# Performance work log

Hardware: AMD Instinct MI355X
Metric: run time of the kernel (lower is better)

Reference implementation:

```python
import jax, jax.numpy as jnp
from jax import lax
import numpy as np

SQRT2 = 1.4142135623730951
STYLE_DIM = 512
MOD_SCALE = 1.0 / np.sqrt(float(STYLE_DIM))          # EqualLinear modulation, lr_mul=1
MAP_SCALE = 0.01 / np.sqrt(float(STYLE_DIM))          # mapping EqualLinear, lr_mul=0.01
LR_MUL = 0.01


def _blur_kernel():
    k = np.array([1.0, 3.0, 3.0, 1.0], dtype=np.float32)
    k = k[None, :] * k[:, None]
    return jnp.asarray(k / k.sum())


def upfirdn2d(x, k, up=1, down=1, pad=(0, 0)):
    # torch upfirdn2d inserts (up-1) zeros AFTER each sample -> extra trailing pad of up-1
    C = x.shape[1]
    kern = jnp.tile(k[None, None], (C, 1, 1, 1))  # depthwise [C,1,kh,kw] (kernel symmetric, no flip needed)
    p = (pad[0], pad[1] + up - 1)
    return lax.conv_general_dilated(x, kern, (down, down), [p, p], lhs_dilation=(up, up),
                                    dimension_numbers=('NCHW', 'OIHW', 'NCHW'), feature_group_count=C)


def fused_lrelu(x, b):
    return jax.nn.leaky_relu(x + b.reshape(1, -1, 1, 1), 0.2) * SQRT2


def grouped_conv(x, w, pad, up):
    # x: [B,I,H,W], w: [B,O,I,k,k] per-sample weights -> grouped conv with B groups
    B, O, I, kh, kw = w.shape
    xg = x.reshape(1, B * I, x.shape[2], x.shape[3])
    if up:
        # torch conv_transpose2d(stride=2, padding=0) == dilated conv with spatially flipped kernel
        wf = jnp.flip(w, (-2, -1)).reshape(B * O, I, kh, kw)
        out = lax.conv_general_dilated(xg, wf, (1, 1), [(kh - 1, kh - 1), (kw - 1, kw - 1)],
                                       lhs_dilation=(2, 2),
                                       dimension_numbers=('NCHW', 'OIHW', 'NCHW'), feature_group_count=B)
    else:
        out = lax.conv_general_dilated(xg, w.reshape(B * O, I, kh, kw), (1, 1), [(pad, pad), (pad, pad)],
                                       dimension_numbers=('NCHW', 'OIHW', 'NCHW'), feature_group_count=B)
    return out.reshape(B, O, out.shape[2], out.shape[3])


def mod_conv(x, weight, style, mod_w, mod_b, demodulate, up, blur_k):
    # weight: [O,I,k,k]; style: [B,512]
    s = style @ (mod_w * MOD_SCALE).T + mod_b                       # [B,I]
    scale = 1.0 / np.sqrt(float(weight.shape[1] * weight.shape[2] * weight.shape[3]))
    w = scale * weight[None] * s[:, None, :, None, None]            # [B,O,I,k,k]
    if demodulate:
        d = lax.rsqrt(jnp.sum(w * w, axis=(2, 3, 4)) + 1e-8)
        w = w * d[:, :, None, None, None]
    out = grouped_conv(x, w, weight.shape[-1] // 2, up)
    if up:
        out = upfirdn2d(out, blur_k * 4.0, pad=(1, 1))              # Blur pad from p=len(k)-2-(3-1)=0
    return out


def _forward(z, mlp_w, mlp_b, const_input, conv_w, conv_mod_w, conv_mod_b, conv_bias,
             noise_strength, rgb_w, rgb_mod_w, rgb_mod_b, rgb_bias):
    B = z.shape[0]
    blur_k = _blur_kernel()
    w_lat = z * lax.rsqrt(jnp.mean(z * z, axis=1, keepdims=True) + 1e-8)
    for i in range(mlp_w.shape[0]):
        w_lat = jax.nn.leaky_relu(w_lat @ (mlp_w[i] * MAP_SCALE).T + mlp_b[i] * LR_MUL, 0.2) * SQRT2
    nkey = jax.random.key(7)

    def noise(l, shape):
        return jax.random.normal(jax.random.fold_in(nkey, l), (shape[0], 1, shape[2], shape[3]), dtype=jnp.float32)

    def styled(x, l, up):
        y = mod_conv(x, conv_w[l], w_lat, conv_mod_w[l], conv_mod_b[l], True, up, blur_k)
        y = y + noise_strength[l] * noise(l, y.shape)
        return fused_lrelu(y, conv_bias[l])

    def to_rgb(x, i):
        y = mod_conv(x, rgb_w[i], w_lat, rgb_mod_w[i], rgb_mod_b[i], False, False, blur_k)
        return y + rgb_bias[i].reshape(1, -1, 1, 1)

    out = jnp.tile(const_input, (B, 1, 1, 1))   # ConstantInput (shift=0 -> identity rolls)
    out = styled(out, 0, False)
    skip = to_rgb(out, 0)
    l = 1
    for blk in range(3):  # resolutions 8, 16, 32
        out = styled(out, l, True); l += 1
        out = styled(out, l, False); l += 1
        # Upsample(skip): kernel*factor^2, pad=(2,1), up=2
        skip = to_rgb(out, blk + 1) + upfirdn2d(skip, blur_k * 4.0, up=2, pad=(2, 1))
    return skip  # [B,3,32,32]


def setup_inputs() -> dict:
    key = jax.random.key(0)
    ks = jax.random.split(key, 8)
    B, S, C = 8, 512, 512
    return {
        'z': jax.random.normal(ks[0], (B, S), jnp.float32),
        'mlp_w': jax.random.normal(ks[1], (8, S, S), jnp.float32),
        'mlp_b': jnp.zeros((8, S), jnp.float32),
        'const_input': jax.random.normal(ks[2], (1, C, 4, 4), jnp.float32),
        'conv_w': jax.random.normal(ks[3], (7, C, C, 3, 3), jnp.float32),
        'conv_mod_w': jax.random.normal(ks[4], (7, C, S), jnp.float32),
        'conv_mod_b': jnp.ones((7, C), jnp.float32),
        'conv_bias': jnp.zeros((7, C), jnp.float32),
        'noise_strength': jax.random.normal(ks[5], (7,), jnp.float32) * 0.1,
        'rgb_w': jax.random.normal(ks[6], (4, 3, C, 1, 1), jnp.float32),
        'rgb_mod_w': jax.random.normal(ks[7], (4, C, S), jnp.float32),
        'rgb_mod_b': jnp.ones((4, C), jnp.float32),
        'rgb_bias': jnp.zeros((4, 3), jnp.float32),
    }


def reference(z, mlp_w, mlp_b, const_input, conv_w, conv_mod_w, conv_mod_b, conv_bias,
              noise_strength, rgb_w, rgb_mod_w, rgb_mod_b, rgb_bias):
    return _forward(z, mlp_w, mlp_b, const_input, conv_w, conv_mod_w, conv_mod_b, conv_bias,
                    noise_strength, rgb_w, rgb_mod_w, rgb_mod_b, rgb_bias)
```

## Files before the change

### kernel.cpp

```cpp
#include <hip/hip_runtime.h>


#define SQRT2F      1.41421356f
#define MAP_SCALE   4.41941738e-04f
#define MOD_SCALE   4.41941738e-02f
#define CONV_SCALE  1.47313913e-02f
#define RGB_SCALE   4.41941738e-02f

typedef __attribute__((ext_vector_type(8))) short bf16x8;
typedef __attribute__((ext_vector_type(16))) float f32x16;

__device__ __forceinline__ float bf2f(ushort u) {
    return __uint_as_float(((unsigned)u) << 16);
}
__device__ __forceinline__ ushort f2bf(float f) {
    unsigned u = __float_as_uint(f);
    unsigned r = (u + 0x7FFFu + ((u >> 16) & 1u)) >> 16;
    return (ushort)r;
}
__device__ __forceinline__ void store4bf(ushort* p, float a, float b, float c, float d) {
    union { ushort u[4]; uint2 v; } x;
    x.u[0] = f2bf(a); x.u[1] = f2bf(b); x.u[2] = f2bf(c); x.u[3] = f2bf(d);
    *(uint2*)p = x.v;
}

typedef __attribute__((address_space(1))) const unsigned int GAS;
typedef __attribute__((address_space(3))) unsigned int LAS;
__device__ __forceinline__ void gload_lds16(const ushort* g, ushort* l) {
    __builtin_amdgcn_global_load_lds((GAS*)g, (LAS*)l, 16, 0, 0);
}


__device__ __forceinline__ unsigned rotl32(unsigned x, int r) {
    return (x << r) | (x >> (32 - r));
}

__device__ void threefry2x32(unsigned k0, unsigned k1, unsigned x0, unsigned x1,
                             unsigned& o0, unsigned& o1) {
    unsigned k2 = k0 ^ k1 ^ 0x1BD11BDAu;
    x0 += k0; x1 += k1;
    x0 += x1; x1 = rotl32(x1,13); x1 ^= x0;
    x0 += x1; x1 = rotl32(x1,15); x1 ^= x0;
    x0 += x1; x1 = rotl32(x1,26); x1 ^= x0;
    x0 += x1; x1 = rotl32(x1, 6); x1 ^= x0;
    x0 += k1; x1 += k2 + 1u;
    x0 += x1; x1 = rotl32(x1,17); x1 ^= x0;
    x0 += x1; x1 = rotl32(x1,29); x1 ^= x0;
    x0 += x1; x1 = rotl32(x1,16); x1 ^= x0;
    x0 += x1; x1 = rotl32(x1,24); x1 ^= x0;
    x0 += k2; x1 += k0 + 2u;
    x0 += x1; x1 = rotl32(x1,13); x1 ^= x0;
    x0 += x1; x1 = rotl32(x1,15); x1 ^= x0;
    x0 += x1; x1 = rotl32(x1,26); x1 ^= x0;
    x0 += x1; x1 = rotl32(x1, 6); x1 ^= x0;
    x0 += k0; x1 += k1 + 3u;
    x0 += x1; x1 = rotl32(x1,17); x1 ^= x0;
    x0 += x1; x1 = rotl32(x1,29); x1 ^= x0;
    x0 += x1; x1 = rotl32(x1,16); x1 ^= x0;
    x0 += x1; x1 = rotl32(x1,24); x1 ^= x0;
    x0 += k1; x1 += k2 + 4u;
    x0 += x1; x1 = rotl32(x1,13); x1 ^= x0;
    x0 += x1; x1 = rotl32(x1,15); x1 ^= x0;
    x0 += x1; x1 = rotl32(x1,26); x1 ^= x0;
    x0 += x1; x1 = rotl32(x1, 6); x1 ^= x0;
    x0 += k2; x1 += k0 + 5u;
    o0 = x0; o1 = x1;
}

__device__ float bits_to_normal(unsigned bits) {
    unsigned m = (bits >> 9) | 0x3F800000u;
    float f = __uint_as_float(m) - 1.0f;
    const float lo = -0.99999994f;
    float u = f * 2.0f + lo;
    u = fmaxf(lo, u);
    float w = -log1pf(-u * u);
    float p;
    if (w < 5.0f) {
        w -= 2.5f;
        p = 2.81022636e-08f;
        p = fmaf(p, w, 3.43273939e-07f);
        p = fmaf(p, w, -3.5233877e-06f);
        p = fmaf(p, w, -4.39150654e-06f);
        p = fmaf(p, w, 0.00021858087f);
        p = fmaf(p, w, -0.00125372503f);
        p = fmaf(p, w, -0.00417768164f);
        p = fmaf(p, w, 0.246640727f);
        p = fmaf(p, w, 1.50140941f);
    } else {
        w = sqrtf(w) - 3.0f;
        p = -0.000200214257f;
        p = fmaf(p, w, 0.000100950558f);
        p = fmaf(p, w, 0.00134934322f);
        p = fmaf(p, w, -0.00367342844f);
        p = fmaf(p, w, 0.00573950773f);
        p = fmaf(p, w, -0.0076224613f);
        p = fmaf(p, w, 0.00943887047f);
        p = fmaf(p, w, 1.00167406f);
        p = fmaf(p, w, 2.83297682f);
    }
    return 1.41421354f * (p * u);
}

__global__ void noise_kernel(float* __restrict__ nbuf) {
    int g = blockIdx.x * 256 + threadIdx.x;
    if (g >= 21632) return;
    const int off[8] = {0, 128, 640, 1152, 3200, 5248, 13440, 21632};
    int l = 0;
    while (l < 6 && g >= off[l + 1]) l++;
    int i = g - off[l];
    unsigned k0, k1;
    threefry2x32(0u, 7u, 0u, (unsigned)l, k0, k1);
    unsigned b0, b1;
    threefry2x32(k0, k1, 0u, (unsigned)i, b0, b1);
    nbuf[g] = bits_to_normal(b0 ^ b1);
}


__global__ void pixelnorm_kernel(const float* __restrict__ z, float* __restrict__ out) {
    int b = blockIdx.x;
    int lane = threadIdx.x;
    float v[8];
    float s = 0.f;
    #pragma unroll
    for (int j = 0; j < 8; j++) {
        v[j] = z[b * 512 + lane + (j << 6)];
        s += v[j] * v[j];
    }
    #pragma unroll
    for (int off = 32; off > 0; off >>= 1) s += __shfl_xor(s, off, 64);
    float norm = rsqrtf(s * (1.f / 512.f) + 1e-8f);
    #pragma unroll
    for (int j = 0; j < 8; j++)
        out[b * 512 + lane + (j << 6)] = v[j] * norm;
}

__global__ void dot512_kernel(const float* __restrict__ win, const float* __restrict__ W,
                              const float* __restrict__ bias, float* __restrict__ out,
                              int total, float wscale, float bscale, int mode) {
    int gt = blockIdx.x * blockDim.x + threadIdx.x;
    int wv = gt >> 6;
    int lane = gt & 63;
    if (wv >= total) return;
    int l = wv >> 12;
    int r = wv & 4095;
    int b = r >> 9;
    int o = r & 511;
    const float* wrow = W + ((size_t)(l * 512 + o) << 9);
    const float* xrow = win + ((size_t)b << 9);
    float s = 0.f;
    #pragma unroll
    for (int j = 0; j < 8; j++) {
        int k = lane + (j << 6);
        s += wrow[k] * xrow[k];
    }
    #pragma unroll
    for (int off = 32; off > 0; off >>= 1) s += __shfl_xor(s, off, 64);
    if (lane == 0) {
        float v = s * wscale + bias[l * 512 + o] * bscale;
        if (mode) v = (v > 0.f ? v : 0.2f * v) * SQRT2F;
        out[wv] = v;
    }
}

__global__ void wbconv_all(const float* __restrict__ cw, ushort* __restrict__ wb7,
                           float* __restrict__ wsq7) {
    int gid = blockIdx.x * 256 + threadIdx.x;
    if (gid >= 7 * 262144) return;
    int l = gid >> 18;
    int idx = gid & 262143;
    int o = idx >> 9, i = idx & 511;
    int flip = (l == 1 || l == 3 || l == 5);
    const float* p = cw + (size_t)gid * 9;
    float w9[9];
    float s = 0.f;
    #pragma unroll
    for (int t = 0; t < 9; t++) { w9[t] = p[t]; s += w9[t] * w9[t]; }
    wsq7[gid] = s;
    ushort* wb = wb7 + (size_t)l * 2359296;
    #pragma unroll
    for (int t = 0; t < 9; t++) {
        int tsrc = flip ? (8 - t) : t;
        wb[((size_t)(t * 512 + o) << 9) + i] = f2bf(w9[tsrc]);
    }
}

__global__ void demod_all(const float* __restrict__ wsq7, const float* __restrict__ sc,
                          float* __restrict__ dm) {
    int gt = blockIdx.x * blockDim.x + threadIdx.x;
    int wv = gt >> 6;
    int lane = gt & 63;
    if (wv >= 7 * 4096) return;
    int l = wv >> 12, b = (wv >> 9) & 7, o = wv & 511;
    const float* wr = wsq7 + (size_t)l * 262144 + ((size_t)o << 9);
    const float* sr = sc + l * 4096 + (b << 9);
    float s = 0.f;
    #pragma unroll
    for (int j = 0; j < 8; j++) {
        int k = lane + (j << 6);
        float sv = sr[k];
        s += wr[k] * sv * sv;
    }
    #pragma unroll
    for (int off = 32; off > 0; off >>= 1) s += __shfl_xor(s, off, 64);
    if (lane == 0) dm[wv] = rsqrtf(s * (1.f / 4608.f) + 1e-8f);
}

__global__ void prep0_kernel(const float* __restrict__ cinp, const float* __restrict__ s0,
                             ushort* __restrict__ X0p) {
    int gid = blockIdx.x * 256 + threadIdx.x;
    if (gid >= 8 * 36 * 64) return;
    int grp = gid & 63;
    int r = gid >> 6;
    int b = r / 36, rc = r % 36, row = rc / 6, col = rc % 6;
    int y = row - 1, x = col - 1;
    union { ushort u[8]; bf16x8 v; } pk;
    if (y >= 0 && y < 4 && x >= 0 && x < 4) {
        #pragma unroll
        for (int k = 0; k < 8; k++) {
            int ch = grp * 8 + k;
            pk.u[k] = f2bf(cinp[ch * 16 + y * 4 + x] * s0[b * 512 + ch]);
        }
    } else {
        #pragma unroll
        for (int k = 0; k < 8; k++) pk.u[k] = 0;
    }
    *(bf16x8*)&X0p[(((size_t)(b * 6 + row) * 6 + col) << 9) + grp * 8] = pk.v;
}

template <int S, int NTILE, int WROWS, int KS, bool WUP>
__global__ __launch_bounds__(256, 2) void conv_dense4(
    const ushort* __restrict__ Xp, const ushort* __restrict__ wb,
    const float* __restrict__ dm, const float* __restrict__ nz,
    const float* __restrict__ nstr, const float* __restrict__ bias,
    const float* __restrict__ snext,
    ushort* __restrict__ T, ushort* __restrict__ XU, float* __restrict__ Pp) {
    constexpr int SP = S + 2, P2 = S * S, N = 8 * P2;
    constexpr int JCOLS = NTILE / 128;
    constexpr int NPX = WROWS * SP;
    constexpr int ASZ = 9 * 4 * 64 * 8;
    constexpr int BSZ = NPX * 32;
    constexpr int PAIR = ASZ + BSZ;
    constexpr int NBU = NPX * 4;
    constexpr int NBT = (NBU + 255) / 256;
    constexpr int ROWMAX = 8 * SP - 1;
    constexpr int CK = 16 / KS;
    constexpr int DB = (CK > 1) ? 2 : 1;
    constexpr int MINB = (NBU > 192) ? ((NBU - 192 + 255) / 256) : 0;
    constexpr int NMIN = 9 + MINB;
    __shared__ __align__(16) ushort lds[DB * PAIR];

    const int tid = threadIdx.x, lane = tid & 63, nw = tid >> 6;
    const int hf = lane >> 5, l31 = lane & 31;
    const int o0 = blockIdx.x * 64;
    const int n0 = blockIdx.y * NTILE;
    const int ks = blockIdx.z;
    const int R0 = (n0 / P2) * SP + (n0 % P2) / S;
    const int ao = tid & 63, ai = tid >> 6;

    int pixbase[JCOLS], nj[JCOLS];
    #pragma unroll
    for (int j = 0; j < JCOLS; j++) {
        int n = n0 + nw * (NTILE / 4) + j * 32 + l31;
        nj[j] = n;
        int b = n / P2, r = n % P2;
        int y = r / S, x = r % S;
        pixbase[j] = (b * SP + y - R0) * SP + x;
    }
    f32x16 acc[JCOLS][2];
    #pragma unroll
    for (int j = 0; j < JCOLS; j++) { acc[j][0] = (f32x16)0.f; acc[j][1] = (f32x16)0.f; }

    int bgo[NBT];
    bool bgv[NBT];
    #pragma unroll
    for (int r = 0; r < NBT; r++) {
        int t = tid + 256 * r;
        bgv[r] = t < NBU;
        int tt = bgv[r] ? t : 0;
        int px = tt % NPX, kv = tt / NPX;
        int rr = px / SP, cc = px % SP;
        int Rc = R0 + rr; if (Rc > ROWMAX) Rc = ROWMAX;
        bgo[r] = ((Rc * SP + cc) << 9) + kv * 8;
    }
    const ushort* wsrc = wb + ((size_t)(o0 + ao) << 9) + ai * 8;
    const int ibase = ks * CK * 32;

    auto stage = [&](int c, int buf) {
        const int i0 = ibase + c * 32;
        ushort* dstA = &lds[buf * PAIR + nw * 512];
        ushort* dstB = &lds[buf * PAIR + ASZ + nw * 512];
        #pragma unroll
        for (int r = 0; r < 9; r++)
            gload_lds16(wsrc + ((size_t)(r * 512) << 9) + i0, dstA + r * 2048);
        #pragma unroll
        for (int r = 0; r < NBT; r++)
            if (bgv[r])
                gload_lds16(Xp + bgo[r] + i0, dstB + r * 2048);
    };

    stage(0, 0);
    for (int c = 0; c < CK; c++) {
        const int cur = c & 1;
        if (c + 1 < CK) {
            stage(c + 1, cur ^ 1);
            asm volatile("s_waitcnt vmcnt(%0)" :: "i"(NMIN) : "memory");
        } else {
            asm volatile("s_waitcnt vmcnt(0)" ::: "memory");
        }
        __builtin_amdgcn_s_barrier();
        __builtin_amdgcn_sched_barrier(0);
        const int bo = cur * PAIR;
        #pragma unroll
        for (int t = 0; t < 9; t++) {
            const int dpx = (t / 3) * SP + (t % 3);
            #pragma unroll
            for (int s = 0; s < 2; s++) {
                const int kv = s * 2 + hf;
                bf16x8 a0 = *(const bf16x8*)&lds[bo + ((t * 4 + kv) * 64 + l31) * 8];
                bf16x8 a1 = *(const bf16x8*)&lds[bo + ((t * 4 + kv) * 64 + 32 + l31) * 8];
                #pragma unroll
                for (int j = 0; j < JCOLS; j++) {
                    bf16x8 bf = *(const bf16x8*)&lds[bo + ASZ + (kv * NPX + pixbase[j] + dpx) * 8];
                    acc[j][0] = __builtin_amdgcn_mfma_f32_32x32x16_bf16(a0, bf, acc[j][0], 0, 0, 0);
                    acc[j][1] = __builtin_amdgcn_mfma_f32_32x32x16_bf16(a1, bf, acc[j][1], 0, 0, 0);
                }
            }
        }
        __builtin_amdgcn_sched_barrier(0);
        __builtin_amdgcn_s_barrier();
    }

    if constexpr (KS > 1) {
        #pragma unroll
        for (int j = 0; j < JCOLS; j++) {
            float* pb = Pp + (((size_t)(ks * N + nj[j])) << 9) + o0;
            #pragma unroll
            for (int sub = 0; sub < 2; sub++) {
                #pragma unroll
                for (int rq = 0; rq < 4; rq++) {
                    float4 v = make_float4(acc[j][sub][rq * 4 + 0], acc[j][sub][rq * 4 + 1],
                                           acc[j][sub][rq * 4 + 2], acc[j][sub][rq * 4 + 3]);
                    *(float4*)&pb[sub * 32 + 4 * hf + 8 * rq] = v;
                }
            }
        }
        return;
    }
    float ns = nstr[0];
    #pragma unroll
    for (int j = 0; j < JCOLS; j++) {
        int n = nj[j], b = n / P2, r = n % P2;
        float nv = nz[b * P2 + r];
        int y = r / S, x = r % S;
        size_t tbase = (size_t)n << 9;
        size_t ubase = ((size_t)(b * SP + y + 1) * SP + x + 1) << 9;
        #pragma unroll
        for (int sub = 0; sub < 2; sub++) {
            #pragma unroll
            for (int rq = 0; rq < 4; rq++) {
                int o = o0 + sub * 32 + 4 * hf + 8 * rq;
                float4 d4 = *(const float4*)&dm[b * 512 + o];
                float4 b4 = *(const float4*)&bias[o];
                float vv[4];
                #pragma unroll
                for (int ri = 0; ri < 4; ri++) {
                    float v = acc[j][sub][rq * 4 + ri] * (&d4.x)[ri] * CONV_SCALE
                              + ns * nv + (&b4.x)[ri];
                    vv[ri] = (v > 0.f ? v : 0.2f * v) * SQRT2F;
                }
                store4bf(T + tbase + o, vv[0], vv[1], vv[2], vv[3]);
                if (WUP) {
                    float4 s4 = *(const float4*)&snext[b * 512 + o];
                    store4bf(XU + ubase + o, vv[0] * s4.x, vv[1] * s4.y,
                             vv[2] * s4.z, vv[3] * s4.w);
                }
            }
        }
    }
}

template <int S, int KS, bool WUP>
__global__ void combine_dense(const float* __restrict__ Pp, const float* __restrict__ dm,
                              const float* __restrict__ nz, const float* __restrict__ nstr,
                              const float* __restrict__ bias, const float* __restrict__ snext,
                              ushort* __restrict__ T, ushort* __restrict__ XU) {
    constexpr int P2 = S * S, N = 8 * P2, SP = S + 2;
    int gid = blockIdx.x * 256 + threadIdx.x;
    int n = gid >> 7, og = (gid & 127) << 2;
    float4 sm = make_float4(0.f, 0.f, 0.f, 0.f);
    #pragma unroll
    for (int k = 0; k < KS; k++) {
        float4 p = *(const float4*)&Pp[(((size_t)(k * N + n)) << 9) + og];
        sm.x += p.x; sm.y += p.y; sm.z += p.z; sm.w += p.w;
    }
    int b = n / P2, r = n % P2;
    float nsv = nstr[0] * nz[b * P2 + r];
    float4 d4 = *(const float4*)&dm[b * 512 + og];
    float4 b4 = *(const float4*)&bias[og];
    float vv[4];
    const float* sp = &sm.x;
    #pragma unroll
    for (int i = 0; i < 4; i++) {
        float v = sp[i] * (&d4.x)[i] * CONV_SCALE + nsv + (&b4.x)[i];
        vv[i] = (v > 0.f ? v : 0.2f * v) * SQRT2F;
    }
    store4bf(&T[((size_t)n << 9) + og], vv[0], vv[1], vv[2], vv[3]);
    if (WUP) {
        int y = r / S, x = r % S;
        float4 s4 = *(const float4*)&snext[b * 512 + og];
        store4bf(&XU[(((size_t)(b * SP + y + 1) * SP + x + 1) << 9) + og],
                 vv[0] * s4.x, vv[1] * s4.y, vv[2] * s4.z, vv[3] * s4.w);
    }
}

template <int HIN, int NTILE, int WRW>
__global__ __launch_bounds__(256, 2) void conv_up4(
    const ushort* __restrict__ Xp, const ushort* __restrict__ wb,
    const float* __restrict__ dm, ushort* __restrict__ U) {
    constexpr int SPI = HIN + 2, SOUT = 2 * HIN + 1, SPO = SOUT + 2;
    constexpr int JCOLS = NTILE / 128;
    constexpr int NPX = WRW * SPI;
    constexpr int ASZ = 4 * 4 * 64 * 8;
    constexpr int BSZ = NPX * 32;
    constexpr int PAIR = ASZ + BSZ;
    constexpr int NBU = NPX * 4;
    constexpr int NBT = (NBU + 255) / 256;
    constexpr int ROWMAX = 8 * SPI - 1;
    constexpr int MINB = (NBU > 192) ? ((NBU - 192 + 255) / 256) : 0;
    constexpr int NMIN = 4 + MINB;
    __shared__ __align__(16) ushort lds[2 * PAIR];

    const int py = blockIdx.z >> 1, pxp = blockIdx.z & 1;
    const int GY = py ? HIN : HIN + 1, GX = pxp ? HIN : HIN + 1;
    const int GG = GY * GX, NCLS = 8 * GG;
    const int NTY = py ? 1 : 2, NTX = pxp ? 1 : 2, NT = NTY * NTX;
    const int n0 = blockIdx.y * NTILE;
    if (n0 >= NCLS) return;

    int taplist[4], toffs[4];
    {
        int k = 0;
        #pragma unroll
        for (int a2 = 0; a2 < 2; a2++) {
            if (a2 >= NTY) break;
            int dy = py ? 1 : a2 * 2;
            #pragma unroll
            for (int c2 = 0; c2 < 2; c2++) {
                if (c2 >= NTX) break;
                int dx = pxp ? 1 : c2 * 2;
                taplist[k] = dy * 3 + dx;
                toffs[k] = ((dy + py) >> 1) * SPI + ((dx + pxp) >> 1);
                k++;
            }
        }
        for (; k < 4; k++) { taplist[k] = 0; toffs[k] = 0; }
    }

    const int tid = threadIdx.x, lane = tid & 63, nw = tid >> 6;
    const int hf = lane >> 5, l31 = lane & 31;
    const int o0 = blockIdx.x * 64;
    const int R0 = (n0 / GG) * SPI + (n0 % GG) / GX;
    const int ao = tid & 63, ai = tid >> 6;

    int pixbase[JCOLS], bj[JCOLS], gyj[JCOLS], gxj[JCOLS];
    bool validj[JCOLS];
    #pragma unroll
    for (int j = 0; j < JCOLS; j++) {
        int n = n0 + nw * (NTILE / 4) + j * 32 + l31;
        validj[j] = n < NCLS;
        int nc = validj[j] ? n : (NCLS - 1);
        int b = nc / GG, rem = nc % GG;
        int gy = rem / GX, gx = rem % GX;
        bj[j] = b; gyj[j] = gy; gxj[j] = gx;
        pixbase[j] = (b * SPI + gy - R0) * SPI + gx;
    }
    f32x16 acc[JCOLS][2];
    #pragma unroll
    for (int j = 0; j < JCOLS; j++) { acc[j][0] = (f32x16)0.f; acc[j][1] = (f32x16)0.f; }

    int bgo[NBT];
    bool bgv[NBT];
    #pragma unroll
    for (int r = 0; r < NBT; r++) {
        int t = tid + 256 * r;
        bgv[r] = t < NBU;
        int tt = bgv[r] ? t : 0;
        int px = tt % NPX, kv = tt / NPX;
        int rr = px / SPI, cc = px % SPI;
        int Rc = R0 + rr; if (Rc > ROWMAX) Rc = ROWMAX;
        bgo[r] = ((Rc * SPI + cc) << 9) + kv * 8;
    }
    const ushort* wsrc = wb + ((size_t)(o0 + ao) << 9) + ai * 8;

    auto stage = [&](int c, int buf) {
        const int i0 = c * 32;
        ushort* dstA = &lds[buf * PAIR + nw * 512];
        ushort* dstB = &lds[buf * PAIR + ASZ + nw * 512];
        #pragma unroll
        for (int r = 0; r < 4; r++)
            gload_lds16(wsrc + ((size_t)(taplist[r] * 512) << 9) + i0, dstA + r * 2048);
        #pragma unroll
        for (int r = 0; r < NBT; r++)
            if (bgv[r])
                gload_lds16(Xp + bgo[r] + i0, dstB + r * 2048);
    };

    stage(0, 0);
    for (int c = 0; c < 16; c++) {
        const int cur = c & 1;
        if (c + 1 < 16) {
            stage(c + 1, cur ^ 1);
            asm volatile("s_waitcnt vmcnt(%0)" :: "i"(NMIN) : "memory");
        } else {
            asm volatile("s_waitcnt vmcnt(0)" ::: "memory");
        }
        __builtin_amdgcn_s_barrier();
        __builtin_amdgcn_sched_barrier(0);
        const int bo = cur * PAIR;
        for (int tt = 0; tt < NT; ++tt) {
            const int dpx = toffs[tt];
            #pragma unroll
            for (int s = 0; s < 2; s++) {
                const int kv = s * 2 + hf;
                bf16x8 a0 = *(const bf16x8*)&lds[bo + ((tt * 4 + kv) * 64 + l31) * 8];
                bf16x8 a1 = *(const bf16x8*)&lds[bo + ((tt * 4 + kv) * 64 + 32 + l31) * 8];
                #pragma unroll
                for (int j = 0; j < JCOLS; j++) {
                    bf16x8 bf = *(const bf16x8*)&lds[bo + ASZ + (kv * NPX + pixbase[j] + dpx) * 8];
                    acc[j][0] = __builtin_amdgcn_mfma_f32_32x32x16_bf16(a0, bf, acc[j][0], 0, 0, 0);
                    acc[j][1] = __builtin_amdgcn_mfma_f32_32x32x16_bf16(a1, bf, acc[j][1], 0, 0, 0);
                }
            }
        }
        __builtin_amdgcn_sched_barrier(0);
        __builtin_amdgcn_s_barrier();
    }
    #pragma unroll
    for (int j = 0; j < JCOLS; j++) {
        if (!validj[j]) continue;
        int b = bj[j];
        int y = 2 * gyj[j] + py, x = 2 * gxj[j] + pxp;
        size_t ubase = ((size_t)(b * SPO + y + 1) * SPO + x + 1) << 9;
        #pragma unroll
        for (int sub = 0; sub < 2; sub++) {
            #pragma unroll
            for (int rq = 0; rq < 4; rq++) {
                int o = o0 + sub * 32 + 4 * hf + 8 * rq;
                float4 d4 = *(const float4*)&dm[b * 512 + o];
                float vv[4];
                #pragma unroll
                for (int ri = 0; ri < 4; ri++)
                    vv[ri] = acc[j][sub][rq * 4 + ri] * (&d4.x)[ri] * CONV_SCALE;
                store4bf(U + ubase + o, vv[0], vv[1], vv[2], vv[3]);
            }
        }
    }
}

template <int SIN>
__global__ void blur_px(const ushort* __restrict__ U, const float* __restrict__ nz,
                        const float* __restrict__ nstr, const float* __restrict__ bias,
                        const float* __restrict__ snext, ushort* __restrict__ X) {
    constexpr int O = SIN - 1, SPI = SIN + 2, SPO = O + 2;
    int gid = blockIdx.x * 256 + threadIdx.x;
    if (gid >= 8 * O * O * 64) return;
    int grp = gid & 63;
    int pxl = gid >> 6;
    int b = pxl / (O * O), r = pxl % (O * O), u = r / O, vcol = r % O;
    const float k1[4] = {0.25f, 0.75f, 0.75f, 0.25f};
    float acc[8];
    #pragma unroll
    for (int k = 0; k < 8; k++) acc[k] = 0.f;
    #pragma unroll
    for (int a = 0; a < 4; a++) {
        int row = b * SPI + u + a;
        #pragma unroll
        for (int c = 0; c < 4; c++) {
            float w = k1[a] * k1[c];
            bf16x8 v = *(const bf16x8*)&U[(((size_t)row * SPI + vcol + c) << 9) + grp * 8];
            #pragma unroll
            for (int k = 0; k < 8; k++) acc[k] += w * bf2f((ushort)v[k]);
        }
    }
    float nsv = nstr[0] * nz[b * O * O + r];
    float4 b0 = *(const float4*)&bias[grp * 8];
    float4 b1 = *(const float4*)&bias[grp * 8 + 4];
    float4 s0 = *(const float4*)&snext[b * 512 + grp * 8];
    float4 s1 = *(const float4*)&snext[b * 512 + grp * 8 + 4];
    union { ushort us[8]; bf16x8 v; } pk;
    #pragma unroll
    for (int k = 0; k < 8; k++) {
        float bk = (k < 4) ? (&b0.x)[k] : (&b1.x)[k - 4];
        float sk = (k < 4) ? (&s0.x)[k] : (&s1.x)[k - 4];
        float v = acc[k] + nsv + bk;
        v = (v > 0.f ? v : 0.2f * v) * SQRT2F;
        pk.us[k] = f2bf(v * sk);
    }
    *(bf16x8*)&X[(((size_t)(b * SPO + u + 1) * SPO + vcol + 1) << 9) + grp * 8] = pk.v;
}

template <int H>
__global__ void skipup_kernel(const float* __restrict__ skip, float* __restrict__ out) {
    constexpr int O = 2 * H;
    int idx = blockIdx.x * 256 + threadIdx.x;
    if (idx >= 8 * 3 * O * O) return;
    int px = idx % (O * O);
    int bc = idx / (O * O);
    int u = px / O, v = px % O;
    const float k1[4] = {0.25f, 0.75f, 0.75f, 0.25f};
    const float* src = skip + (size_t)bc * (H * H);
    float acc = 0.f;
    #pragma unroll
    for (int ty = 0; ty < 4; ty++) {
        int r = u + ty - 2;
        if (r < 0 || (r & 1) || (r >> 1) >= H) continue;
        float rsum = 0.f;
        #pragma unroll
        for (int tx = 0; tx < 4; tx++) {
            int cc = v + tx - 2;
            if (cc < 0 || (cc & 1) || (cc >> 1) >= H) continue;
            rsum += k1[tx] * src[(r >> 1) * H + (cc >> 1)];
        }
        acc += k1[ty] * rsum;
    }
    out[(size_t)bc * (O * O) + px] = acc;
}

__global__ void torgb_px(const ushort* __restrict__ T, int P2,
                         const float* __restrict__ rgbw, const float* __restrict__ srgb,
                         const float* __restrict__ rbias, const float* __restrict__ skipup,
                         float* __restrict__ dst) {
    int b = blockIdx.x;
    int px = blockIdx.y * 4 + (threadIdx.x >> 6);
    int lane = threadIdx.x & 63;
    int c8 = lane * 8;
    bf16x8 v = *(const bf16x8*)&T[(((size_t)b * P2 + px) << 9) + c8];
    float4 sa = *(const float4*)&srgb[b * 512 + c8];
    float4 sb = *(const float4*)&srgb[b * 512 + c8 + 4];
    float xs[8];
    #pragma unroll
    for (int k = 0; k < 8; k++) {
        float sk = (k < 4) ? (&sa.x)[k] : (&sb.x)[k - 4];
        xs[k] = bf2f((ushort)v[k]) * sk;
    }
    float sums[3];
    #pragma unroll
    for (int c = 0; c < 3; c++) {
        float4 w0 = *(const float4*)&rgbw[c * 512 + c8];
        float4 w1 = *(const float4*)&rgbw[c * 512 + c8 + 4];
        float s = 0.f;
        #pragma unroll
        for (int k = 0; k < 8; k++) {
            float wk = (k < 4) ? (&w0.x)[k] : (&w1.x)[k - 4];
            s += xs[k] * wk;
        }
        #pragma unroll
        for (int off = 32; off > 0; off >>= 1) s += __shfl_xor(s, off, 64);
        sums[c] = s;
    }
    if (lane == 0) {
        #pragma unroll
        for (int c = 0; c < 3; c++) {
            float o = sums[c] * RGB_SCALE + rbias[c];
            if (skipup) o += skipup[((size_t)b * 3 + c) * P2 + px];
            dst[((size_t)b * 3 + c) * P2 + px] = o;
        }
    }
}


extern "C" void kernel_launch(void* const* d_in, const int* in_sizes, int n_in,
                              void* d_out, int out_size, void* d_ws, size_t ws_size,
                              hipStream_t stream) {
    const float* z      = (const float*)d_in[0];
    const float* mlp_w  = (const float*)d_in[1];
    const float* mlp_b  = (const float*)d_in[2];
    const float* cinp   = (const float*)d_in[3];
    const float* conv_w = (const float*)d_in[4];
    const float* cmw    = (const float*)d_in[5];
    const float* cmb    = (const float*)d_in[6];
    const float* cbias  = (const float*)d_in[7];
    const float* nstr   = (const float*)d_in[8];
    const float* rgbw   = (const float*)d_in[9];
    const float* rmw    = (const float*)d_in[10];
    const float* rmb    = (const float*)d_in[11];
    const float* rbias  = (const float*)d_in[12];
    float* out = (float*)d_out;
    float* ws = (float*)d_ws;

    float* wlatA = ws;
    float* wlatB = ws + 4096;
    float* sconv = ws + 8192;
    float* srgb  = ws + 36864;
    float* dem   = ws + 53248;
    float* noise = ws + 81920;
    float* skipA = ws + 103552;
    float* skipB = ws + 128128;
    float* skipU = ws + 152704;
    float* wsq7  = ws + 177280;
    ushort* wbuf7 = (ushort*)(ws + 2012288);
    float* Ppart = ws + 10269824;
    ushort* A1 = (ushort*)(ws + 12366976);
    ushort* A2 = (ushort*)(ws + 14875776);
    ushort* A3 = (ushort*)(ws + 17243264);

    ushort* X0p = A1;
    ushort* T0  = A2;
    ushort* XU1 = A3;
    ushort* U1  = A1;
    ushort* X2  = A2;
    ushort* T2  = A3;
    ushort* XU3 = A1;
    ushort* U3  = A2;
    ushort* X4  = A1;
    ushort* T4  = A2;
    ushort* XU5 = A3;
    ushort* U5  = A1;
    ushort* X6  = A2;
    ushort* T6  = A3;

    const size_t LWB = 2359296;

    wbconv_all<<<7168, 256, 0, stream>>>(conv_w, wbuf7, wsq7);
    noise_kernel<<<85, 256, 0, stream>>>(noise);

    pixelnorm_kernel<<<8, 64, 0, stream>>>(z, wlatA);
    float* a = wlatA;
    float* bb = wlatB;
    for (int i = 0; i < 8; i++) {
        dot512_kernel<<<1024, 256, 0, stream>>>(a, mlp_w + (size_t)i * 262144,
                                                mlp_b + i * 512, bb, 4096,
                                                MAP_SCALE, 0.01f, 1);
        float* t = a; a = bb; bb = t;
    }
    dot512_kernel<<<7168, 256, 0, stream>>>(a, cmw, cmb, sconv, 7 * 4096, MOD_SCALE, 1.0f, 0);
    dot512_kernel<<<4096, 256, 0, stream>>>(a, rmw, rmb, srgb, 4 * 4096, MOD_SCALE, 1.0f, 0);
    demod_all<<<7168, 256, 0, stream>>>(wsq7, sconv, dem);
    prep0_kernel<<<72, 256, 0, stream>>>(cinp, sconv, X0p);

    conv_dense4<4, 128, 48, 16, false><<<dim3(8, 1, 16), 256, 0, stream>>>(
        X0p, wbuf7, nullptr, nullptr, nullptr, nullptr, nullptr,
        nullptr, nullptr, Ppart);
    hipMemsetAsync(XU1, 0, (size_t)8 * 36 * 512 * 2, stream);
    combine_dense<4, 16, true><<<64, 256, 0, stream>>>(
        Ppart, dem, noise, nstr, cbias, sconv + 4096, T0, XU1);
    torgb_px<<<dim3(8, 4), 256, 0, stream>>>(T0, 16, rgbw, srgb, rbias, nullptr, skipA);

    hipMemsetAsync(U1, 0, (size_t)8 * 121 * 512 * 2, stream);
    conv_up4<4, 128, 48><<<dim3(8, 2, 4), 256, 0, stream>>>(XU1, wbuf7 + LWB, dem + 4096, U1);
    hipMemsetAsync(X2, 0, (size_t)8 * 100 * 512 * 2, stream);
    blur_px<9><<<128, 256, 0, stream>>>(U1, noise + 128, nstr + 1, cbias + 512,
                                        sconv + 2 * 4096, X2);

    conv_dense4<8, 128, 20, 8, false><<<dim3(8, 4, 8), 256, 0, stream>>>(
        X2, wbuf7 + 2 * LWB, nullptr, nullptr, nullptr, nullptr, nullptr,
        nullptr, nullptr, Ppart);
    hipMemsetAsync(XU3, 0, (size_t)8 * 100 * 512 * 2, stream);
    combine_dense<8, 8, true><<<256, 256, 0, stream>>>(
        Ppart, dem + 2 * 4096, noise + 640, nstr + 2, cbias + 2 * 512,
        sconv + 3 * 4096, T2, XU3);
    skipup_kernel<4><<<6, 256, 0, stream>>>(skipA, skipU);
    torgb_px<<<dim3(8, 16), 256, 0, stream>>>(T2, 64, rgbw + 1536, srgb + 4096,
                                              rbias + 3, skipU, skipB);

    hipMemsetAsync(U3, 0, (size_t)8 * 361 * 512 * 2, stream);
    conv_up4<8, 128, 22><<<dim3(8, 6, 4), 256, 0, stream>>>(XU3, wbuf7 + 3 * LWB,
                                                            dem + 3 * 4096, U3);
    hipMemsetAsync(X4, 0, (size_t)8 * 324 * 512 * 2, stream);
    blur_px<17><<<512, 256, 0, stream>>>(U3, noise + 1152, nstr + 3, cbias + 3 * 512,
                                         sconv + 4 * 4096, X4);

    conv_dense4<16, 128, 10, 2, false><<<dim3(8, 16, 2), 256, 0, stream>>>(
        X4, wbuf7 + 4 * LWB, nullptr, nullptr, nullptr, nullptr, nullptr,
        nullptr, nullptr, Ppart);
    hipMemsetAsync(XU5, 0, (size_t)8 * 324 * 512 * 2, stream);
    combine_dense<16, 2, true><<<1024, 256, 0, stream>>>(
        Ppart, dem + 4 * 4096, noise + 3200, nstr + 4, cbias + 4 * 512,
        sconv + 5 * 4096, T4, XU5);
    skipup_kernel<8><<<24, 256, 0, stream>>>(skipB, skipU);
    torgb_px<<<dim3(8, 64), 256, 0, stream>>>(T4, 256, rgbw + 2 * 1536, srgb + 2 * 4096,
                                              rbias + 6, skipU, skipA);

    hipMemsetAsync(U5, 0, (size_t)8 * 1225 * 512 * 2, stream);
    conv_up4<16, 256, 20><<<dim3(8, 10, 4), 256, 0, stream>>>(XU5, wbuf7 + 5 * LWB,
                                                              dem + 5 * 4096, U5);
    hipMemsetAsync(X6, 0, (size_t)8 * 1156 * 512 * 2, stream);
    blur_px<33><<<2048, 256, 0, stream>>>(U5, noise + 5248, nstr + 5, cbias + 5 * 512,
                                          sconv + 6 * 4096, X6);

    conv_dense4<32, 256, 10, 1, false><<<dim3(8, 32, 1), 256, 0, stream>>>(
        X6, wbuf7 + 6 * LWB, dem + 6 * 4096, noise + 13440, nstr + 6, cbias + 6 * 512,
        nullptr, T6, nullptr, nullptr);
    skipup_kernel<16><<<96, 256, 0, stream>>>(skipA, skipU);
    torgb_px<<<dim3(8, 256), 256, 0, stream>>>(T6, 1024, rgbw + 3 * 1536, srgb + 3 * 4096,
                                               rbias + 9, skipU, out);
}
```

Measured before the change: 459.9 us.

## Re-layout weights and activations into channel-group-major blocks for contiguous staging loads

Changes the bf16 weight buffer and the padded activation buffers from pixel-major with 512 interleaved channels to a blocked layout. Channels are split into groups of 8, with each group (and each 32-channel chunk) laid out contiguously across pixels. Every producer (weight prep, prep0, combine, conv epilogues, blur) and consumer (conv_dense, conv_up staging) is updated to match. The goal is more contiguous global-to-LDS loads per k-chunk, replacing the 1 KB-strided 16-byte gathers. In exchange, epilogue stores become scattered 8-byte writes, since each 8-channel group now lives in a separate plane.

Measured after the change: 427.6 us. -7.0%, faster.

```diff
diff --git a/kernel.cpp b/kernel.cpp
--- a/kernel.cpp
+++ b/kernel.cpp
@@ -177,10 +177,11 @@
     for (int t = 0; t < 9; t++) { w9[t] = p[t]; s += w9[t] * w9[t]; }
     wsq7[gid] = s;
     ushort* wb = wb7 + (size_t)l * 2359296;
+    int c = i >> 5, kv = (i >> 3) & 3, e = i & 7;
     #pragma unroll
     for (int t = 0; t < 9; t++) {
         int tsrc = flip ? (8 - t) : t;
-        wb[((size_t)(t * 512 + o) << 9) + i] = f2bf(w9[tsrc]);
+        wb[(size_t)(((c * 9 + t) * 4 + kv) * 512 + o) * 8 + e] = f2bf(w9[tsrc]);
     }
 }
 
@@ -224,17 +225,18 @@
         #pragma unroll
         for (int k = 0; k < 8; k++) pk.u[k] = 0;
     }
-    *(bf16x8*)&X0p[(((size_t)(b * 6 + row) * 6 + col) << 9) + grp * 8] = pk.v;
+    *(bf16x8*)&X0p[((size_t)grp * 288 + r) * 8] = pk.v;
 }
 
 template <int S, int NTILE, int WROWS, int KS, bool WUP>
-__global__ __launch_bounds__(256, 2) void conv_dense4(
+__global__ __launch_bounds__(256, 2) void conv_dense5(
     const ushort* __restrict__ Xp, const ushort* __restrict__ wb,
     const float* __restrict__ dm, const float* __restrict__ nz,
     const float* __restrict__ nstr, const float* __restrict__ bias,
     const float* __restrict__ snext,
     ushort* __restrict__ T, ushort* __restrict__ XU, float* __restrict__ Pp) {
     constexpr int SP = S + 2, P2 = S * S, N = 8 * P2;
+    constexpr int PXT = 8 * SP * SP;
     constexpr int JCOLS = NTILE / 128;
     constexpr int NPX = WROWS * SP;
     constexpr int ASZ = 9 * 4 * 64 * 8;
@@ -255,7 +257,6 @@
     const int n0 = blockIdx.y * NTILE;
     const int ks = blockIdx.z;
     const int R0 = (n0 / P2) * SP + (n0 % P2) / S;
-    const int ao = tid & 63, ai = tid >> 6;
 
     int pixbase[JCOLS], nj[JCOLS];
     #pragma unroll
@@ -280,29 +281,29 @@
         int px = tt % NPX, kv = tt / NPX;
         int rr = px / SP, cc = px % SP;
         int Rc = R0 + rr; if (Rc > ROWMAX) Rc = ROWMAX;
-        bgo[r] = ((Rc * SP + cc) << 9) + kv * 8;
-    }
-    const ushort* wsrc = wb + ((size_t)(o0 + ao) << 9) + ai * 8;
-    const int ibase = ks * CK * 32;
-
-    auto stage = [&](int c, int buf) {
-        const int i0 = ibase + c * 32;
+        bgo[r] = (kv * PXT + Rc * SP + cc) * 8;
+    }
+    const int aoff = (nw * 512 + o0 + lane) * 8;
+
+    auto stage = [&](int cgi, int buf) {
         ushort* dstA = &lds[buf * PAIR + nw * 512];
         ushort* dstB = &lds[buf * PAIR + ASZ + nw * 512];
+        const ushort* asrc = wb + (size_t)cgi * 147456 + aoff;
         #pragma unroll
         for (int r = 0; r < 9; r++)
-            gload_lds16(wsrc + ((size_t)(r * 512) << 9) + i0, dstA + r * 2048);
+            gload_lds16(asrc + r * 16384, dstA + r * 2048);
+        const ushort* bsrc = Xp + (size_t)cgi * (PXT * 32);
         #pragma unroll
         for (int r = 0; r < NBT; r++)
             if (bgv[r])
-                gload_lds16(Xp + bgo[r] + i0, dstB + r * 2048);
+                gload_lds16(bsrc + bgo[r], dstB + r * 2048);
     };
 
-    stage(0, 0);
+    stage(ks * CK, 0);
     for (int c = 0; c < CK; c++) {
         const int cur = c & 1;
         if (c + 1 < CK) {
-            stage(c + 1, cur ^ 1);
+            stage(ks * CK + c + 1, cur ^ 1);
             asm volatile("s_waitcnt vmcnt(%0)" :: "i"(NMIN) : "memory");
         } else {
             asm volatile("s_waitcnt vmcnt(0)" ::: "memory");
@@ -353,7 +354,7 @@
         float nv = nz[b * P2 + r];
         int y = r / S, x = r % S;
         size_t tbase = (size_t)n << 9;
-        size_t ubase = ((size_t)(b * SP + y + 1) * SP + x + 1) << 9;
+        int gpx = (b * SP + y + 1) * SP + x + 1;
         #pragma unroll
         for (int sub = 0; sub < 2; sub++) {
             #pragma unroll
@@ -371,8 +372,8 @@
                 store4bf(T + tbase + o, vv[0], vv[1], vv[2], vv[3]);
                 if (WUP) {
                     float4 s4 = *(const float4*)&snext[b * 512 + o];
-                    store4bf(XU + ubase + o, vv[0] * s4.x, vv[1] * s4.y,
-                             vv[2] * s4.z, vv[3] * s4.w);
+                    store4bf(XU + ((size_t)(o >> 3) * PXT + gpx) * 8 + (o & 7),
+                             vv[0] * s4.x, vv[1] * s4.y, vv[2] * s4.z, vv[3] * s4.w);
                 }
             }
         }
@@ -385,6 +386,7 @@
                               const float* __restrict__ bias, const float* __restrict__ snext,
                               ushort* __restrict__ T, ushort* __restrict__ XU) {
     constexpr int P2 = S * S, N = 8 * P2, SP = S + 2;
+    constexpr int PXT = 8 * SP * SP;
     int gid = blockIdx.x * 256 + threadIdx.x;
     int n = gid >> 7, og = (gid & 127) << 2;
     float4 sm = make_float4(0.f, 0.f, 0.f, 0.f);
@@ -407,17 +409,20 @@
     store4bf(&T[((size_t)n << 9) + og], vv[0], vv[1], vv[2], vv[3]);
     if (WUP) {
         int y = r / S, x = r % S;
+        int gpx = (b * SP + y + 1) * SP + x + 1;
         float4 s4 = *(const float4*)&snext[b * 512 + og];
-        store4bf(&XU[(((size_t)(b * SP + y + 1) * SP + x + 1) << 9) + og],
+        store4bf(&XU[((size_t)(og >> 3) * PXT + gpx) * 8 + (og & 7)],
                  vv[0] * s4.x, vv[1] * s4.y, vv[2] * s4.z, vv[3] * s4.w);
     }
 }
 
 template <int HIN, int NTILE, int WRW>
-__global__ __launch_bounds__(256, 2) void conv_up4(
+__global__ __launch_bounds__(256, 2) void conv_up5(
     const ushort* __restrict__ Xp, const ushort* __restrict__ wb,
     const float* __restrict__ dm, ushort* __restrict__ U) {
     constexpr int SPI = HIN + 2, SOUT = 2 * HIN + 1, SPO = SOUT + 2;
+    constexpr int PXT = 8 * SPI * SPI;
+    constexpr int PXTO = 8 * SPO * SPO;
     constexpr int JCOLS = NTILE / 128;
     constexpr int NPX = WRW * SPI;
     constexpr int ASZ = 4 * 4 * 64 * 8;
@@ -460,7 +465,6 @@
     const int hf = lane >> 5, l31 = lane & 31;
     const int o0 = blockIdx.x * 64;
     const int R0 = (n0 / GG) * SPI + (n0 % GG) / GX;
-    const int ao = tid & 63, ai = tid >> 6;
 
     int pixbase[JCOLS], bj[JCOLS], gyj[JCOLS], gxj[JCOLS];
     bool validj[JCOLS];
@@ -488,21 +492,25 @@
         int px = tt % NPX, kv = tt / NPX;
         int rr = px / SPI, cc = px % SPI;
         int Rc = R0 + rr; if (Rc > ROWMAX) Rc = ROWMAX;
-        bgo[r] = ((Rc * SPI + cc) << 9) + kv * 8;
-    }
-    const ushort* wsrc = wb + ((size_t)(o0 + ao) << 9) + ai * 8;
-
-    auto stage = [&](int c, int buf) {
-        const int i0 = c * 32;
+        bgo[r] = (kv * PXT + Rc * SPI + cc) * 8;
+    }
+    const int aoff = (nw * 512 + o0 + lane) * 8;
+    int atap[4];
+    #pragma unroll
+    for (int r = 0; r < 4; r++) atap[r] = taplist[r] * 16384;
+
+    auto stage = [&](int cgi, int buf) {
         ushort* dstA = &lds[buf * PAIR + nw * 512];
         ushort* dstB = &lds[buf * PAIR + ASZ + nw * 512];
+        const ushort* asrc = wb + (size_t)cgi * 147456 + aoff;
         #pragma unroll
         for (int r = 0; r < 4; r++)
-            gload_lds16(wsrc + ((size_t)(taplist[r] * 512) << 9) + i0, dstA + r * 2048);
+            gload_lds16(asrc + atap[r], dstA + r * 2048);
+        const ushort* bsrc = Xp + (size_t)cgi * (PXT * 32);
         #pragma unroll
         for (int r = 0; r < NBT; r++)
             if (bgv[r])
-                gload_lds16(Xp + bgo[r] + i0, dstB + r * 2048);
+                gload_lds16(bsrc + bgo[r], dstB + r * 2048);
     };
 
     stage(0, 0);
@@ -540,7 +548,7 @@
         if (!validj[j]) continue;
         int b = bj[j];
         int y = 2 * gyj[j] + py, x = 2 * gxj[j] + pxp;
-        size_t ubase = ((size_t)(b * SPO + y + 1) * SPO + x + 1) << 9;
+        int gpx = (b * SPO + y + 1) * SPO + x + 1;
         #pragma unroll
         for (int sub = 0; sub < 2; sub++) {
             #pragma unroll
@@ -551,7 +559,8 @@
                 #pragma unroll
                 for (int ri = 0; ri < 4; ri++)
                     vv[ri] = acc[j][sub][rq * 4 + ri] * (&d4.x)[ri] * CONV_SCALE;
-                store4bf(U + ubase + o, vv[0], vv[1], vv[2], vv[3]);
+                store4bf(U + ((size_t)(o >> 3) * PXTO + gpx) * 8 + (o & 7),
+                         vv[0], vv[1], vv[2], vv[3]);
             }
         }
     }
@@ -562,6 +571,8 @@
                         const float* __restrict__ nstr, const float* __restrict__ bias,
                         const float* __restrict__ snext, ushort* __restrict__ X) {
     constexpr int O = SIN - 1, SPI = SIN + 2, SPO = O + 2;
+    constexpr int PXTU = 8 * SPI * SPI;
+    constexpr int PXTO = 8 * SPO * SPO;
     int gid = blockIdx.x * 256 + threadIdx.x;
     if (gid >= 8 * O * O * 64) return;
     int grp = gid & 63;
@@ -571,13 +582,14 @@
     float acc[8];
     #pragma unroll
     for (int k = 0; k < 8; k++) acc[k] = 0.f;
+    const ushort* Ug = U + (size_t)grp * PXTU * 8;
     #pragma unroll
     for (int a = 0; a < 4; a++) {
         int row = b * SPI + u + a;
         #pragma unroll
         for (int c = 0; c < 4; c++) {
             float w = k1[a] * k1[c];
-            bf16x8 v = *(const bf16x8*)&U[(((size_t)row * SPI + vcol + c) << 9) + grp * 8];
+            bf16x8 v = *(const bf16x8*)&Ug[(size_t)(row * SPI + vcol + c) * 8];
             #pragma unroll
             for (int k = 0; k < 8; k++) acc[k] += w * bf2f((ushort)v[k]);
         }
@@ -596,7 +608,7 @@
         v = (v > 0.f ? v : 0.2f * v) * SQRT2F;
         pk.us[k] = f2bf(v * sk);
     }
-    *(bf16x8*)&X[(((size_t)(b * SPO + u + 1) * SPO + vcol + 1) << 9) + grp * 8] = pk.v;
+    *(bf16x8*)&X[((size_t)grp * PXTO + (b * SPO + u + 1) * SPO + vcol + 1) * 8] = pk.v;
 }
 
 template <int H>
@@ -738,7 +750,7 @@
     demod_all<<<7168, 256, 0, stream>>>(wsq7, sconv, dem);
     prep0_kernel<<<72, 256, 0, stream>>>(cinp, sconv, X0p);
 
-    conv_dense4<4, 128, 48, 16, false><<<dim3(8, 1, 16), 256, 0, stream>>>(
+    conv_dense5<4, 128, 48, 16, false><<<dim3(8, 1, 16), 256, 0, stream>>>(
         X0p, wbuf7, nullptr, nullptr, nullptr, nullptr, nullptr,
         nullptr, nullptr, Ppart);
     hipMemsetAsync(XU1, 0, (size_t)8 * 36 * 512 * 2, stream);
@@ -747,12 +759,12 @@
     torgb_px<<<dim3(8, 4), 256, 0, stream>>>(T0, 16, rgbw, srgb, rbias, nullptr, skipA);
 
     hipMemsetAsync(U1, 0, (size_t)8 * 121 * 512 * 2, stream);
-    conv_up4<4, 128, 48><<<dim3(8, 2, 4), 256, 0, stream>>>(XU1, wbuf7 + LWB, dem + 4096, U1);
+    conv_up5<4, 128, 48><<<dim3(8, 2, 4), 256, 0, stream>>>(XU1, wbuf7 + LWB, dem + 4096, U1);
     hipMemsetAsync(X2, 0, (size_t)8 * 100 * 512 * 2, stream);
     blur_px<9><<<128, 256, 0, stream>>>(U1, noise + 128, nstr + 1, cbias + 512,
                                         sconv + 2 * 4096, X2);
 
-    conv_dense4<8, 128, 20, 8, false><<<dim3(8, 4, 8), 256, 0, stream>>>(
+    conv_dense5<8, 128, 20, 8, false><<<dim3(8, 4, 8), 256, 0, stream>>>(
         X2, wbuf7 + 2 * LWB, nullptr, nullptr, nullptr, nullptr, nullptr,
         nullptr, nullptr, Ppart);
     hipMemsetAsync(XU3, 0, (size_t)8 * 100 * 512 * 2, stream);
@@ -764,13 +776,13 @@
                                               rbias + 3, skipU, skipB);
 
     hipMemsetAsync(U3, 0, (size_t)8 * 361 * 512 * 2, stream);
-    conv_up4<8, 128, 22><<<dim3(8, 6, 4), 256, 0, stream>>>(XU3, wbuf7 + 3 * LWB,
+    conv_up5<8, 128, 22><<<dim3(8, 6, 4), 256, 0, stream>>>(XU3, wbuf7 + 3 * LWB,
                                                             dem + 3 * 4096, U3);
     hipMemsetAsync(X4, 0, (size_t)8 * 324 * 512 * 2, stream);
     blur_px<17><<<512, 256, 0, stream>>>(U3, noise + 1152, nstr + 3, cbias + 3 * 512,
                                          sconv + 4 * 4096, X4);
 
-    conv_dense4<16, 128, 10, 2, false><<<dim3(8, 16, 2), 256, 0, stream>>>(
+    conv_dense5<16, 128, 10, 2, false><<<dim3(8, 16, 2), 256, 0, stream>>>(
         X4, wbuf7 + 4 * LWB, nullptr, nullptr, nullptr, nullptr, nullptr,
         nullptr, nullptr, Ppart);
     hipMemsetAsync(XU5, 0, (size_t)8 * 324 * 512 * 2, stream);
@@ -782,13 +794,13 @@
                                               rbias + 6, skipU, skipA);
 
     hipMemsetAsync(U5, 0, (size_t)8 * 1225 * 512 * 2, stream);
-    conv_up4<16, 256, 20><<<dim3(8, 10, 4), 256, 0, stream>>>(XU5, wbuf7 + 5 * LWB,
+    conv_up5<16, 256, 20><<<dim3(8, 10, 4), 256, 0, stream>>>(XU5, wbuf7 + 5 * LWB,
                                                               dem + 5 * 4096, U5);
     hipMemsetAsync(X6, 0, (size_t)8 * 1156 * 512 * 2, stream);
     blur_px<33><<<2048, 256, 0, stream>>>(U5, noise + 5248, nstr + 5, cbias + 5 * 512,
                                           sconv + 6 * 4096, X6);
 
-    conv_dense4<32, 256, 10, 1, false><<<dim3(8, 32, 1), 256, 0, stream>>>(
+    conv_dense5<32, 256, 10, 1, false><<<dim3(8, 32, 1), 256, 0, stream>>>(
         X6, wbuf7 + 6 * LWB, dem + 6 * 4096, noise + 13440, nstr + 6, cbias + 6 * 512,
         nullptr, T6, nullptr, nullptr);
     skipup_kernel<16><<<96, 256, 0, stream>>>(skipA, skipU);
```
